# Kernel optimization log

Measured on AMD Instinct MI355X. Metric: run time of the kernel, lower is better.

## Reference

```python
import jax, jax.numpy as jnp
import numpy as np

B, N, C = 2, 2048, 768
H = 12
HD = C // H  # 64
EPS = 1e-6


def setup_inputs() -> dict:
    key = jax.random.key(0)
    ks = jax.random.split(key, 6)
    x = jax.random.normal(ks[0], (B, N, C), dtype=jnp.float32)
    # Xavier-uniform-ish init for kernels
    lim_qkv = float(np.sqrt(6.0 / (C + 3 * C)))
    lim_proj = float(np.sqrt(6.0 / (C + C)))
    qkv_kernel = jax.random.uniform(ks[1], (C, 3 * C), minval=-lim_qkv, maxval=lim_qkv, dtype=jnp.float32)
    qkv_bias = jnp.zeros((3 * C,), dtype=jnp.float32)
    proj_kernel = jax.random.uniform(ks[2], (C, C), minval=-lim_proj, maxval=lim_proj, dtype=jnp.float32)
    proj_bias = jnp.zeros((C,), dtype=jnp.float32)
    q_norm_w = jnp.ones((HD,), dtype=jnp.float32)
    k_norm_w = jnp.ones((HD,), dtype=jnp.float32)
    # Standard RoPE tables: freqs over half the head dim, tiled to full head_dim
    half = HD // 2
    inv_freq = 1.0 / (10000.0 ** (jnp.arange(0, half, dtype=jnp.float32) / half))
    t = jnp.arange(N, dtype=jnp.float32)
    freqs = jnp.outer(t, inv_freq)               # (N, HD/2)
    emb = jnp.concatenate([freqs, freqs], axis=-1)  # (N, HD)
    rope_cos = jnp.cos(emb)
    rope_sin = jnp.sin(emb)
    return {"x": x, "rope_cos": rope_cos, "rope_sin": rope_sin,
            "qkv_kernel": qkv_kernel, "qkv_bias": qkv_bias,
            "proj_kernel": proj_kernel, "proj_bias": proj_bias,
            "q_norm_w": q_norm_w, "k_norm_w": k_norm_w}


def _rms_norm(x, w):
    var = jnp.mean(x * x, axis=-1, keepdims=True)
    return x * jax.lax.rsqrt(var + EPS) * w


def _rope(x, cos, sin):
    # x: (B, H, N, HD); cos/sin: (N, HD)
    half = x.shape[-1] // 2
    x1, x2 = x[..., :half], x[..., half:]
    rot = jnp.concatenate([-x2, x1], axis=-1)
    return x * cos + rot * sin


def reference(x, rope_cos, rope_sin, qkv_kernel, qkv_bias, proj_kernel, proj_bias, q_norm_w, k_norm_w):
    b, n, c = x.shape
    qkv = x @ qkv_kernel + qkv_bias                       # (B, N, 3C)
    qkv = qkv.reshape(b, n, 3, H, HD).transpose(2, 0, 3, 1, 4)  # (3, B, H, N, HD)
    q, k, v = qkv[0], qkv[1], qkv[2]
    q = _rope(_rms_norm(q, q_norm_w), rope_cos, rope_sin)
    k = _rope(_rms_norm(k, k_norm_w), rope_cos, rope_sin)
    scale = 1.0 / jnp.sqrt(jnp.float32(HD)).astype(x.dtype)
    attn = jnp.einsum('bhqd,bhkd->bhqk', q, k) * scale    # (B, H, N, N)
    attn = jax.nn.softmax(attn, axis=-1)
    out = jnp.einsum('bhqk,bhkd->bhqd', attn, v)          # (B, H, N, HD)
    out = out.swapaxes(1, 2).reshape(b, n, c)
    return out @ proj_kernel + proj_bias
```

## Files before the change

### kernel.cpp

```cpp
#include <hip/hip_runtime.h>
#include <math.h>

#define B_    2
#define N_    2048
#define C_    768
#define H_    12
#define HD_   64
#define NROWS (B_*N_)
#define QKVC  (3*C_)
#define EPSV  1e-6f
#define SCALE 0.125f
#define LOG2E 1.44269504088896f
#define SMAX  12.0f

typedef unsigned short u16;
typedef short bf16x8 __attribute__((ext_vector_type(8)));
typedef float f32x4  __attribute__((ext_vector_type(4)));

__device__ __forceinline__ float b2f(u16 u) {
    unsigned v = ((unsigned)u) << 16;
    return __builtin_bit_cast(float, v);
}
__device__ __forceinline__ u16 f2b(float f) {
    unsigned u = __builtin_bit_cast(unsigned, f);
    u += 0x7fffu + ((u >> 16) & 1u);
    return (u16)(u >> 16);
}
__device__ __forceinline__ unsigned pk2(float a, float b) {
#if __has_builtin(__builtin_amdgcn_cvt_pk_bf16_f32)
    auto r = __builtin_amdgcn_cvt_pk_bf16_f32(a, b);
    return __builtin_bit_cast(unsigned, r);
#else
    return (unsigned)f2b(a) | ((unsigned)f2b(b) << 16);
#endif
}
__device__ __forceinline__ float fexp2(float x) {
#if __has_builtin(__builtin_amdgcn_exp2f)
    return __builtin_amdgcn_exp2f(x);
#else
    return exp2f(x);
#endif
}
__device__ __forceinline__ void gload_lds16(const void* g, void* l) {
    __builtin_amdgcn_global_load_lds(
        (const __attribute__((address_space(1))) unsigned int*)g,
        (__attribute__((address_space(3))) unsigned int*)l, 16, 0, 0);
}

__global__ __launch_bounds__(256)
void cvt_bf16_kernel(const float* __restrict__ src, u16* __restrict__ dst) {
    const int i = (blockIdx.x * 256 + threadIdx.x) * 4;
    const float4 v = *(const float4*)(src + i);
    uint2 o = { pk2(v.x, v.y), pk2(v.z, v.w) };
    *(uint2*)(dst + i) = o;
}

__global__ __launch_bounds__(256)
void wtrans_kernel(const float* __restrict__ W, u16* __restrict__ Wt,
                   int K, int N) {
    __shared__ float T[64][65];
    const int k0 = blockIdx.y * 64, n0 = blockIdx.x * 64;
    const int t = threadIdx.x, r = t >> 6, c = t & 63;
#pragma unroll
    for (int p = 0; p < 16; ++p) {
        const int kl = p * 4 + r;
        T[kl][c] = W[(size_t)(k0 + kl) * N + n0 + c];
    }
    __syncthreads();
#pragma unroll
    for (int p = 0; p < 16; ++p) {
        const int nl = p * 4 + r;
        Wt[(size_t)(n0 + nl) * K + k0 + c] = f2b(T[c][nl]);
    }
}

template <bool BF16OUT, int BN>
__global__ __launch_bounds__(256)
void gemm_tn_kernel(const u16* __restrict__ A, const u16* __restrict__ Bt,
                    const float* __restrict__ bias, void* __restrict__ Cout,
                    int M, int N, int K) {
    constexpr int NB = BN / 32;
    __shared__ __attribute__((aligned(16))) u16 As[128 * 32];
    __shared__ __attribute__((aligned(16))) u16 Bs[BN * 32];
    const int tid = threadIdx.x;
    const int w = tid >> 6, l = tid & 63;
    const int lq = l & 15, quad = l >> 4;

    const int gx  = gridDim.x;
    const int nwg = gx * gridDim.y;
    const int d   = blockIdx.x + gx * blockIdx.y;
    const int lin = (d & 7) * (nwg >> 3) + (d >> 3);
    const int mbase = (lin / gx) * 128, nbase = (lin % gx) * BN;

    f32x4 acc[4][NB];
    const f32x4 z4 = {0.f, 0.f, 0.f, 0.f};
#pragma unroll
    for (int mb = 0; mb < 4; ++mb)
#pragma unroll
        for (int nb = 0; nb < NB; ++nb) acc[mb][nb] = z4;

    const int srow = (l >> 2);
    const int sdc  = (l & 3) ^ ((l >> 2) & 3);

    for (int k0 = 0; k0 < K; k0 += 32) {
#pragma unroll
        for (int cc = 0; cc < 2; ++cc) {
            const int c = 2 * w + cc;
            const int row = 16 * c + srow;
            gload_lds16(A + (size_t)(mbase + row) * K + k0 + sdc * 8, &As[c * 512]);
        }
#pragma unroll
        for (int cc = 0; cc < BN / 64; ++cc) {
            const int c = (BN / 64) * w + cc;
            const int row = 16 * c + srow;
            gload_lds16(Bt + (size_t)(nbase + row) * K + k0 + sdc * 8, &Bs[c * 512]);
        }
        __syncthreads();

        bf16x8 af[4], bfr[NB];
#pragma unroll
        for (int mb = 0; mb < 4; ++mb)
            af[mb] = *(const bf16x8*)
                &As[((w >> 1) * 64 + mb * 16 + lq) * 32 + ((quad ^ (lq & 3)) * 8)];
#pragma unroll
        for (int nb = 0; nb < NB; ++nb)
            bfr[nb] = *(const bf16x8*)
                &Bs[((w & 1) * (BN / 2) + nb * 16 + lq) * 32 + ((quad ^ (lq & 3)) * 8)];
#pragma unroll
        for (int mb = 0; mb < 4; ++mb)
#pragma unroll
            for (int nb = 0; nb < NB; ++nb)
                acc[mb][nb] = __builtin_amdgcn_mfma_f32_16x16x32_bf16(
                    af[mb], bfr[nb], acc[mb][nb], 0, 0, 0);
        __syncthreads();
    }

#pragma unroll
    for (int nb = 0; nb < NB; ++nb) {
        const int col = nbase + (w & 1) * (BN / 2) + nb * 16 + lq;
        const float bv = bias[col];
#pragma unroll
        for (int mb = 0; mb < 4; ++mb) {
#pragma unroll
            for (int r = 0; r < 4; ++r) {
                const int row = mbase + (w >> 1) * 64 + mb * 16 + quad * 4 + r;
                const float v = acc[mb][nb][r] + bv;
                if (BF16OUT) ((u16*)Cout)[(size_t)row * N + col] = f2b(v);
                else         ((float*)Cout)[(size_t)row * N + col] = v;
            }
        }
    }
}

__global__ __launch_bounds__(256)
void normrope_kernel(u16* __restrict__ qkv, u16* __restrict__ kpack,
                     const float* __restrict__ cosb,
                     const float* __restrict__ sinb,
                     const float* __restrict__ qw,
                     const float* __restrict__ kw) {
    const int item = blockIdx.x * 16 + (threadIdx.x >> 4);
    const int lq   = threadIdx.x & 15;
    const int h    = item % H_;
    const int row  = item / H_;
    const int n    = row & (N_ - 1);
    const int b    = row >> 11;
    const size_t base = (size_t)row * QKVC + h * HD_ + lq * 4;

    const ushort4 q4 = *(const ushort4*)&qkv[base];
    const ushort4 k4 = *(const ushort4*)&qkv[base + C_];
    float qf[4], kf[4];
    qf[0] = b2f(q4.x); qf[1] = b2f(q4.y); qf[2] = b2f(q4.z); qf[3] = b2f(q4.w);
    kf[0] = b2f(k4.x); kf[1] = b2f(k4.y); kf[2] = b2f(k4.z); kf[3] = b2f(k4.w);

    float q2 = qf[0]*qf[0] + qf[1]*qf[1] + qf[2]*qf[2] + qf[3]*qf[3];
    float k2 = kf[0]*kf[0] + kf[1]*kf[1] + kf[2]*kf[2] + kf[3]*kf[3];
#pragma unroll
    for (int off = 8; off >= 1; off >>= 1) {
        q2 += __shfl_xor(q2, off, 64);
        k2 += __shfl_xor(k2, off, 64);
    }
    const float rq = rsqrtf(q2 * (1.f / 64.f) + EPSV);
    const float rk = rsqrtf(k2 * (1.f / 64.f) + EPSV);

    const float4 qwv = *(const float4*)&qw[lq * 4];
    const float4 kwv = *(const float4*)&kw[lq * 4];
    const float4 cv  = *(const float4*)&cosb[n * HD_ + lq * 4];
    const float4 sv  = *(const float4*)&sinb[n * HD_ + lq * 4];

    float qn[4], kn[4];
    qn[0] = qf[0]*rq*qwv.x; qn[1] = qf[1]*rq*qwv.y;
    qn[2] = qf[2]*rq*qwv.z; qn[3] = qf[3]*rq*qwv.w;
    kn[0] = kf[0]*rk*kwv.x; kn[1] = kf[1]*rk*kwv.y;
    kn[2] = kf[2]*rk*kwv.z; kn[3] = kf[3]*rk*kwv.w;

    const float sgn = (lq < 8) ? -1.f : 1.f;
    float qo[4], ko[4];
    const float cc[4] = {cv.x, cv.y, cv.z, cv.w};
    const float ss[4] = {sv.x, sv.y, sv.z, sv.w};
#pragma unroll
    for (int j = 0; j < 4; ++j) {
        const float qp = __shfl_xor(qn[j], 8, 64);
        const float kp = __shfl_xor(kn[j], 8, 64);
        qo[j] = (qn[j] * cc[j] + sgn * qp * ss[j]) * (SCALE * LOG2E);
        ko[j] =  kn[j] * cc[j] + sgn * kp * ss[j];
    }
    uint2 qout = { pk2(qo[0], qo[1]), pk2(qo[2], qo[3]) };
    uint2 kout = { pk2(ko[0], ko[1]), pk2(ko[2], ko[3]) };
    *(uint2*)&qkv[base] = qout;

    const int kt = n >> 6, kr = n & 63;
    const int kb = kr >> 4, m = kr & 15;
    const int ks = lq >> 3, quad = (lq >> 1) & 3, jj = (lq & 1) * 4;
    const size_t off = ((size_t)(b * H_ + h) * 32 + kt) * 4096
                     + (size_t)((kb * 2 + ks) * 64 + quad * 16 + m) * 8 + jj;
    *(uint2*)&kpack[off] = kout;
}

__global__ __launch_bounds__(256)
void vpack_kernel(const u16* __restrict__ qkv, u16* __restrict__ vpack) {
    __shared__ u16 Tv[64][72];
    const int kt = blockIdx.x, bh = blockIdx.y;
    const int b = bh / H_, h = bh % H_;
    const int t = threadIdx.x;
    {
        const int r = t >> 2, seg = t & 3;
        const u16* src = &qkv[(size_t)(b * N_ + kt * 64 + r) * QKVC
                              + 2 * C_ + h * HD_ + seg * 16];
        const uint4 v0 = *(const uint4*)src;
        const uint4 v1 = *(const uint4*)(src + 8);
        *(uint4*)&Tv[r][seg * 16]     = v0;
        *(uint4*)&Tv[r][seg * 16 + 8] = v1;
    }
    __syncthreads();
    u16 tmp[16];
#pragma unroll
    for (int g2 = 0; g2 < 2; ++g2) {
        const int g = t * 2 + g2;
        const int mbks = g >> 6;
        const int l  = g & 63;
        const int mb = mbks >> 1, ks = mbks & 1;
        const int m  = l & 15,  quad = l >> 4;
#pragma unroll
        for (int j = 0; j < 8; ++j)
            tmp[g2 * 8 + j] = Tv[ks * 32 + quad * 8 + j][mb * 16 + m];
    }
    u16* dst = &vpack[((size_t)bh * 32 + kt) * 4096 + t * 16];
    *(uint4*)dst       = *(const uint4*)&tmp[0];
    *(uint4*)(dst + 8) = *(const uint4*)&tmp[8];
}

#define NQ_   2
#define QB_   (NQ_ * 16)
#define NQT_  (N_ / QB_)

__global__ __launch_bounds__(128, 3)
void flash_mfma_kernel(const u16* __restrict__ qkv,
                       const u16* __restrict__ kpack,
                       const u16* __restrict__ vpack,
                       u16* __restrict__ attnb) {
    __shared__ __attribute__((aligned(16))) u16 Ps[2][QB_ * 64];
    __shared__ __attribute__((aligned(16))) float Oex[QB_ * 64];
    __shared__ float lex[QB_];

    const int tid = threadIdx.x;
    const int w = tid >> 6, l = tid & 63;
    const int lq = l & 15, quad = l >> 4;
    const int sw = lq & 7;

    const int lin  = blockIdx.x;
    const int slot = lin >> 3;
    const int bh   = (lin & 7) * 3 + (slot / NQT_);
    const int qt   = slot & (NQT_ - 1);
    const int b = bh / H_, h = bh % H_;
    const size_t qbase = (size_t)b * N_ * QKVC + h * HD_;
    const size_t tbase = (size_t)bh * 32 * 4096;

    bf16x8 qb[NQ_][2];
#pragma unroll
    for (int nq = 0; nq < NQ_; ++nq)
#pragma unroll
        for (int ks = 0; ks < 2; ++ks)
            qb[nq][ks] = *(const bf16x8*)
                &qkv[qbase + (size_t)(qt * QB_ + nq * 16 + lq) * QKVC
                     + ks * 32 + quad * 8];

    float lsum[NQ_];
#pragma unroll
    for (int nq = 0; nq < NQ_; ++nq) lsum[nq] = 0.f;
    f32x4 oacc[4][NQ_];
    const f32x4 z4 = {0.f, 0.f, 0.f, 0.f};
#pragma unroll
    for (int mb = 0; mb < 4; ++mb)
#pragma unroll
        for (int nq = 0; nq < NQ_; ++nq) oacc[mb][nq] = z4;

    bf16x8 ka[4][2];
#pragma unroll
    for (int kb = 0; kb < 4; ++kb)
#pragma unroll
        for (int ks = 0; ks < 2; ++ks)
            ka[kb][ks] = *(const bf16x8*)
                &kpack[tbase + (size_t)w * 4096 + ((kb * 2 + ks) * 64 + l) * 8];

    for (int kt2 = 0; kt2 < 16; ++kt2) {
        const int kt  = 2 * kt2 + w;
        const int ktn = (kt + 2) & 31;
        const size_t vb = tbase + (size_t)kt * 4096;
        const size_t kb_n = tbase + (size_t)ktn * 4096;

        bf16x8 va[4][2];
#pragma unroll
        for (int mb = 0; mb < 4; ++mb)
#pragma unroll
            for (int ks = 0; ks < 2; ++ks)
                va[mb][ks] = *(const bf16x8*)
                    &vpack[vb + ((mb * 2 + ks) * 64 + l) * 8];

#pragma unroll
        for (int kb = 0; kb < 4; ++kb) {
            f32x4 sacc[NQ_];
#pragma unroll
            for (int nq = 0; nq < NQ_; ++nq) sacc[nq] = z4;
            __builtin_amdgcn_s_setprio(1);
#pragma unroll
            for (int ks = 0; ks < 2; ++ks)
#pragma unroll
                for (int nq = 0; nq < NQ_; ++nq)
                    sacc[nq] = __builtin_amdgcn_mfma_f32_16x16x32_bf16(
                        ka[kb][ks], qb[nq][ks], sacc[nq], 0, 0, 0);
            __builtin_amdgcn_s_setprio(0);
#pragma unroll
            for (int nq = 0; nq < NQ_; ++nq) {
                float p[4];
#pragma unroll
                for (int r = 0; r < 4; ++r) p[r] = fexp2(sacc[nq][r] - SMAX);
                lsum[nq] += (p[0] + p[1]) + (p[2] + p[3]);
                uint2 pkv = { pk2(p[0], p[1]), pk2(p[2], p[3]) };
                *(uint2*)&Ps[w][(nq * 16 + lq) * 64
                                + (((kb * 2 + (quad >> 1)) ^ sw) * 8)
                                + (quad & 1) * 4] = pkv;
            }
        }

#pragma unroll
        for (int kb = 0; kb < 4; ++kb)
#pragma unroll
            for (int ks = 0; ks < 2; ++ks)
                ka[kb][ks] = *(const bf16x8*)
                    &kpack[kb_n + ((kb * 2 + ks) * 64 + l) * 8];

        bf16x8 pb[2][NQ_];
#pragma unroll
        for (int ks = 0; ks < 2; ++ks)
#pragma unroll
            for (int nq = 0; nq < NQ_; ++nq)
                pb[ks][nq] = *(const bf16x8*)
                    &Ps[w][(nq * 16 + lq) * 64 + (((ks * 4 + quad) ^ sw) * 8)];

        __builtin_amdgcn_s_setprio(1);
#pragma unroll
        for (int mb = 0; mb < 4; ++mb)
#pragma unroll
            for (int ks = 0; ks < 2; ++ks)
#pragma unroll
                for (int nq = 0; nq < NQ_; ++nq)
                    oacc[mb][nq] = __builtin_amdgcn_mfma_f32_16x16x32_bf16(
                        va[mb][ks], pb[ks][nq], oacc[mb][nq], 0, 0, 0);
        __builtin_amdgcn_s_setprio(0);
    }

#pragma unroll
    for (int nq = 0; nq < NQ_; ++nq) {
        lsum[nq] += __shfl_xor(lsum[nq], 16, 64);
        lsum[nq] += __shfl_xor(lsum[nq], 32, 64);
    }

    if (w == 1) {
#pragma unroll
        for (int nq = 0; nq < NQ_; ++nq) {
#pragma unroll
            for (int mb = 0; mb < 4; ++mb) {
                const int chunk = (mb * 4 + quad) ^ lq;
                *(float4*)&Oex[(nq * 16 + lq) * 64 + chunk * 4] =
                    *(float4*)&oacc[mb][nq];
            }
            if (quad == 0) lex[nq * 16 + lq] = lsum[nq];
        }
    }
    __syncthreads();
    if (w == 0) {
#pragma unroll
        for (int nq = 0; nq < NQ_; ++nq) {
            const int qrow = nq * 16 + lq;
            const float inv = 1.f / (lsum[nq] + lex[qrow]);
#pragma unroll
            for (int mb = 0; mb < 4; ++mb) {
                const int chunk = (mb * 4 + quad) ^ lq;
                const float4 oe = *(const float4*)&Oex[qrow * 64 + chunk * 4];
                const float o0 = (oacc[mb][nq][0] + oe.x) * inv;
                const float o1 = (oacc[mb][nq][1] + oe.y) * inv;
                const float o2 = (oacc[mb][nq][2] + oe.z) * inv;
                const float o3 = (oacc[mb][nq][3] + oe.w) * inv;
                uint2 ov = { pk2(o0, o1), pk2(o2, o3) };
                *(uint2*)&Ps[0][qrow * 64
                                + (((mb * 2 + (quad >> 1)) ^ sw) * 8)
                                + (quad & 1) * 4] = ov;
            }
        }
#pragma unroll
        for (int pass = 0; pass < QB_ / 8; ++pass) {
            const int ql = pass * 8 + (l >> 3);
            const int c  = l & 7;
            const bf16x8 v = *(const bf16x8*)&Ps[0][ql * 64 + ((c ^ (ql & 7)) * 8)];
            const int query = qt * QB_ + ql;
            *(bf16x8*)&attnb[(size_t)(b * N_ + query) * C_ + h * HD_ + c * 8] = v;
        }
    }
}

extern "C" void kernel_launch(void* const* d_in, const int* in_sizes, int n_in,
                              void* d_out, int out_size, void* d_ws, size_t ws_size,
                              hipStream_t stream) {
    const float* x        = (const float*)d_in[0];
    const float* rope_cos = (const float*)d_in[1];
    const float* rope_sin = (const float*)d_in[2];
    const float* qkv_w    = (const float*)d_in[3];
    const float* qkv_b    = (const float*)d_in[4];
    const float* proj_w   = (const float*)d_in[5];
    const float* proj_b   = (const float*)d_in[6];
    const float* q_nw     = (const float*)d_in[7];
    const float* k_nw     = (const float*)d_in[8];
    float* out = (float*)d_out;

    u16* xb    = (u16*)d_ws;
    u16* qwt   = xb    + (size_t)NROWS * C_;
    u16* pwt   = qwt   + (size_t)QKVC * C_;
    u16* qkvb  = pwt   + (size_t)C_ * C_;
    u16* vpackb= qkvb  + (size_t)NROWS * QKVC;
    u16* attnb = vpackb+ (size_t)B_ * H_ * 32 * 4096;
    u16* kpackb= xb;

    cvt_bf16_kernel<<<dim3(NROWS * C_ / 1024), 256, 0, stream>>>(x, xb);
    wtrans_kernel<<<dim3(QKVC / 64, C_ / 64), 256, 0, stream>>>(qkv_w, qwt, C_, QKVC);
    wtrans_kernel<<<dim3(C_ / 64, C_ / 64), 256, 0, stream>>>(proj_w, pwt, C_, C_);

    gemm_tn_kernel<true, 128><<<dim3(QKVC / 128, NROWS / 128), 256, 0, stream>>>(
        xb, qwt, qkv_b, qkvb, NROWS, QKVC, C_);

    normrope_kernel<<<dim3(NROWS * H_ / 16), 256, 0, stream>>>(
        qkvb, kpackb, rope_cos, rope_sin, q_nw, k_nw);

    vpack_kernel<<<dim3(32, B_ * H_), 256, 0, stream>>>(qkvb, vpackb);

    flash_mfma_kernel<<<dim3(B_ * H_ * NQT_), 128, 0, stream>>>(
        qkvb, kpackb, vpackb, attnb);

    gemm_tn_kernel<false, 64><<<dim3(C_ / 64, NROWS / 128), 256, 0, stream>>>(
        attnb, pwt, proj_b, out, NROWS, C_, C_);
}
```

Before: 180.4 us.

## Merge prep and norm/vpack launches; double-buffer K tiles in flash loop

Folds the three preprocessing kernels (x cast plus two weight transposes) into one launch, and the normrope and vpack kernels into one launch, with work routed by block-index ranges. This removes launch gaps and lets independent small jobs share the GPU at once. The flash attention loop now keeps K fragments in a two-slot register buffer and issues the next tile's K load before the QK MFMAs, so the load can overlap compute. The cost is more vector registers per wave, which may reduce occupancy under the 3-blocks-per-SM launch bound.

```diff
diff --git a/kernel.cpp b/kernel.cpp
--- a/kernel.cpp
+++ b/kernel.cpp
@@ -47,19 +47,11 @@
         (__attribute__((address_space(3))) unsigned int*)l, 16, 0, 0);
 }
 
-__global__ __launch_bounds__(256)
-void cvt_bf16_kernel(const float* __restrict__ src, u16* __restrict__ dst) {
-    const int i = (blockIdx.x * 256 + threadIdx.x) * 4;
-    const float4 v = *(const float4*)(src + i);
-    uint2 o = { pk2(v.x, v.y), pk2(v.z, v.w) };
-    *(uint2*)(dst + i) = o;
-}
-
-__global__ __launch_bounds__(256)
-void wtrans_kernel(const float* __restrict__ W, u16* __restrict__ Wt,
-                   int K, int N) {
-    __shared__ float T[64][65];
-    const int k0 = blockIdx.y * 64, n0 = blockIdx.x * 64;
+__device__ __forceinline__ void wtrans_body(const float* __restrict__ W,
+                                            u16* __restrict__ Wt,
+                                            int K, int N, int bx, int by,
+                                            float (*T)[65]) {
+    const int k0 = by * 64, n0 = bx * 64;
     const int t = threadIdx.x, r = t >> 6, c = t & 63;
 #pragma unroll
     for (int p = 0; p < 16; ++p) {
@@ -71,6 +63,25 @@
     for (int p = 0; p < 16; ++p) {
         const int nl = p * 4 + r;
         Wt[(size_t)(n0 + nl) * K + k0 + c] = f2b(T[c][nl]);
+    }
+}
+
+__global__ __launch_bounds__(256)
+void prep_kernel(const float* __restrict__ x, u16* __restrict__ xb,
+                 const float* __restrict__ qkv_w, u16* __restrict__ qwt,
+                 const float* __restrict__ proj_w, u16* __restrict__ pwt) {
+    __shared__ float T[64][65];
+    const int blk = blockIdx.x;
+    if (blk < 432) {
+        wtrans_body(qkv_w, qwt, C_, QKVC, blk % 36, blk / 36, T);
+    } else if (blk < 576) {
+        const int lin = blk - 432;
+        wtrans_body(proj_w, pwt, C_, C_, lin % 12, lin / 12, T);
+    } else {
+        const int i = ((blk - 576) * 256 + threadIdx.x) * 4;
+        const float4 v = *(const float4*)(x + i);
+        uint2 o = { pk2(v.x, v.y), pk2(v.z, v.w) };
+        *(uint2*)(xb + i) = o;
     }
 }
 
@@ -152,13 +163,12 @@
     }
 }
 
-__global__ __launch_bounds__(256)
-void normrope_kernel(u16* __restrict__ qkv, u16* __restrict__ kpack,
-                     const float* __restrict__ cosb,
-                     const float* __restrict__ sinb,
-                     const float* __restrict__ qw,
-                     const float* __restrict__ kw) {
-    const int item = blockIdx.x * 16 + (threadIdx.x >> 4);
+__device__ __forceinline__ void normrope_body(
+        u16* __restrict__ qkv, u16* __restrict__ kpack,
+        const float* __restrict__ cosb, const float* __restrict__ sinb,
+        const float* __restrict__ qw, const float* __restrict__ kw,
+        int blk) {
+    const int item = blk * 16 + (threadIdx.x >> 4);
     const int lq   = threadIdx.x & 15;
     const int h    = item % H_;
     const int row  = item / H_;
@@ -216,10 +226,9 @@
     *(uint2*)&kpack[off] = kout;
 }
 
-__global__ __launch_bounds__(256)
-void vpack_kernel(const u16* __restrict__ qkv, u16* __restrict__ vpack) {
-    __shared__ u16 Tv[64][72];
-    const int kt = blockIdx.x, bh = blockIdx.y;
+__device__ __forceinline__ void vpack_body(
+        const u16* __restrict__ qkv, u16* __restrict__ vpack,
+        int kt, int bh, u16 (*Tv)[72]) {
     const int b = bh / H_, h = bh % H_;
     const int t = threadIdx.x;
     {
@@ -249,6 +258,22 @@
     *(uint4*)(dst + 8) = *(const uint4*)&tmp[8];
 }
 
+__global__ __launch_bounds__(256)
+void normvpack_kernel(u16* __restrict__ qkv, u16* __restrict__ kpack,
+                      u16* __restrict__ vpack,
+                      const float* __restrict__ cosb,
+                      const float* __restrict__ sinb,
+                      const float* __restrict__ qw,
+                      const float* __restrict__ kw) {
+    __shared__ u16 Tv[64][72];
+    const int blk = blockIdx.x;
+    if (blk < 768) {
+        vpack_body(qkv, vpack, blk & 31, blk >> 5, Tv);
+    } else {
+        normrope_body(qkv, kpack, cosb, sinb, qw, kw, blk - 768);
+    }
+}
+
 #define NQ_   2
 #define QB_   (NQ_ * 16)
 #define NQT_  (N_ / QB_)
@@ -294,80 +319,89 @@
 #pragma unroll
         for (int nq = 0; nq < NQ_; ++nq) oacc[mb][nq] = z4;
 
-    bf16x8 ka[4][2];
+    bf16x8 ka[2][4][2];
 #pragma unroll
     for (int kb = 0; kb < 4; ++kb)
 #pragma unroll
         for (int ks = 0; ks < 2; ++ks)
-            ka[kb][ks] = *(const bf16x8*)
+            ka[0][kb][ks] = *(const bf16x8*)
                 &kpack[tbase + (size_t)w * 4096 + ((kb * 2 + ks) * 64 + l) * 8];
 
-    for (int kt2 = 0; kt2 < 16; ++kt2) {
-        const int kt  = 2 * kt2 + w;
-        const int ktn = (kt + 2) & 31;
-        const size_t vb = tbase + (size_t)kt * 4096;
-        const size_t kb_n = tbase + (size_t)ktn * 4096;
-
-        bf16x8 va[4][2];
-#pragma unroll
-        for (int mb = 0; mb < 4; ++mb)
-#pragma unroll
-            for (int ks = 0; ks < 2; ++ks)
-                va[mb][ks] = *(const bf16x8*)
-                    &vpack[vb + ((mb * 2 + ks) * 64 + l) * 8];
-
-#pragma unroll
-        for (int kb = 0; kb < 4; ++kb) {
-            f32x4 sacc[NQ_];
-#pragma unroll
-            for (int nq = 0; nq < NQ_; ++nq) sacc[nq] = z4;
-            __builtin_amdgcn_s_setprio(1);
-#pragma unroll
-            for (int ks = 0; ks < 2; ++ks)
-#pragma unroll
-                for (int nq = 0; nq < NQ_; ++nq)
-                    sacc[nq] = __builtin_amdgcn_mfma_f32_16x16x32_bf16(
-                        ka[kb][ks], qb[nq][ks], sacc[nq], 0, 0, 0);
-            __builtin_amdgcn_s_setprio(0);
-#pragma unroll
-            for (int nq = 0; nq < NQ_; ++nq) {
-                float p[4];
-#pragma unroll
-                for (int r = 0; r < 4; ++r) p[r] = fexp2(sacc[nq][r] - SMAX);
-                lsum[nq] += (p[0] + p[1]) + (p[2] + p[3]);
-                uint2 pkv = { pk2(p[0], p[1]), pk2(p[2], p[3]) };
-                *(uint2*)&Ps[w][(nq * 16 + lq) * 64
-                                + (((kb * 2 + (quad >> 1)) ^ sw) * 8)
-                                + (quad & 1) * 4] = pkv;
-            }
-        }
-
-#pragma unroll
-        for (int kb = 0; kb < 4; ++kb)
-#pragma unroll
-            for (int ks = 0; ks < 2; ++ks)
-                ka[kb][ks] = *(const bf16x8*)
-                    &kpack[kb_n + ((kb * 2 + ks) * 64 + l) * 8];
-
-        bf16x8 pb[2][NQ_];
-#pragma unroll
-        for (int ks = 0; ks < 2; ++ks)
-#pragma unroll
-            for (int nq = 0; nq < NQ_; ++nq)
-                pb[ks][nq] = *(const bf16x8*)
-                    &Ps[w][(nq * 16 + lq) * 64 + (((ks * 4 + quad) ^ sw) * 8)];
-
-        __builtin_amdgcn_s_setprio(1);
-#pragma unroll
-        for (int mb = 0; mb < 4; ++mb)
-#pragma unroll
-            for (int ks = 0; ks < 2; ++ks)
-#pragma unroll
-                for (int nq = 0; nq < NQ_; ++nq)
-                    oacc[mb][nq] = __builtin_amdgcn_mfma_f32_16x16x32_bf16(
-                        va[mb][ks], pb[ks][nq], oacc[mb][nq], 0, 0, 0);
-        __builtin_amdgcn_s_setprio(0);
-    }
+    int kt2i = 0;
+
+#define FLASH_ITER(P)                                                         \
+    do {                                                                      \
+        const int kt  = 2 * kt2i + w;                                         \
+        const int ktn = (kt + 2) & 31;         \
+        const size_t vb   = tbase + (size_t)kt * 4096;                        \
+        const size_t kb_n = tbase + (size_t)ktn * 4096;                       \
+             \
+        bf16x8 va[4][2];                                                      \
+        _Pragma("unroll")                                                     \
+        for (int mb = 0; mb < 4; ++mb)                                        \
+            _Pragma("unroll")                                                 \
+            for (int ks = 0; ks < 2; ++ks)                                    \
+                va[mb][ks] = *(const bf16x8*)                                 \
+                    &vpack[vb + ((mb * 2 + ks) * 64 + l) * 8];                \
+        _Pragma("unroll")                                                     \
+        for (int kb = 0; kb < 4; ++kb)                                        \
+            _Pragma("unroll")                                                 \
+            for (int ks = 0; ks < 2; ++ks)                                    \
+                ka[1 - (P)][kb][ks] = *(const bf16x8*)                        \
+                    &kpack[kb_n + ((kb * 2 + ks) * 64 + l) * 8];              \
+                                      \
+        _Pragma("unroll")                                                     \
+        for (int kb = 0; kb < 4; ++kb) {                                      \
+            f32x4 sacc[NQ_];                                                  \
+            _Pragma("unroll")                                                 \
+            for (int nq = 0; nq < NQ_; ++nq) sacc[nq] = z4;                   \
+            __builtin_amdgcn_s_setprio(1);                                    \
+            _Pragma("unroll")                                                 \
+            for (int ks = 0; ks < 2; ++ks)                                    \
+                _Pragma("unroll")                                             \
+                for (int nq = 0; nq < NQ_; ++nq)                              \
+                    sacc[nq] = __builtin_amdgcn_mfma_f32_16x16x32_bf16(       \
+                        ka[(P)][kb][ks], qb[nq][ks], sacc[nq], 0, 0, 0);      \
+            __builtin_amdgcn_s_setprio(0);                                    \
+            _Pragma("unroll")                                                 \
+            for (int nq = 0; nq < NQ_; ++nq) {                                \
+                float p[4];                                                   \
+                _Pragma("unroll")                                             \
+                for (int r = 0; r < 4; ++r) p[r] = fexp2(sacc[nq][r] - SMAX); \
+                lsum[nq] += (p[0] + p[1]) + (p[2] + p[3]);                    \
+                uint2 pkv = { pk2(p[0], p[1]), pk2(p[2], p[3]) };             \
+                *(uint2*)&Ps[w][(nq * 16 + lq) * 64                           \
+                                + (((kb * 2 + (quad >> 1)) ^ sw) * 8)         \
+                                + (quad & 1) * 4] = pkv;                      \
+            }                                                                 \
+        }                                                                     \
+              \
+        bf16x8 pb[2][NQ_];                                                    \
+        _Pragma("unroll")                                                     \
+        for (int ks = 0; ks < 2; ++ks)                                        \
+            _Pragma("unroll")                                                 \
+            for (int nq = 0; nq < NQ_; ++nq)                                  \
+                pb[ks][nq] = *(const bf16x8*)                                 \
+                    &Ps[w][(nq * 16 + lq) * 64 + (((ks * 4 + quad) ^ sw) * 8)];\
+                                                          \
+        __builtin_amdgcn_s_setprio(1);                                        \
+        _Pragma("unroll")                                                     \
+        for (int mb = 0; mb < 4; ++mb)                                        \
+            _Pragma("unroll")                                                 \
+            for (int ks = 0; ks < 2; ++ks)                                    \
+                _Pragma("unroll")                                             \
+                for (int nq = 0; nq < NQ_; ++nq)                              \
+                    oacc[mb][nq] = __builtin_amdgcn_mfma_f32_16x16x32_bf16(   \
+                        va[mb][ks], pb[ks][nq], oacc[mb][nq], 0, 0, 0);       \
+        __builtin_amdgcn_s_setprio(0);                                        \
+        ++kt2i;                                                               \
+    } while (0)
+
+    for (int it8 = 0; it8 < 8; ++it8) {
+        FLASH_ITER(0);
+        FLASH_ITER(1);
+    }
+#undef FLASH_ITER
 
 #pragma unroll
     for (int nq = 0; nq < NQ_; ++nq) {
@@ -440,17 +474,14 @@
     u16* attnb = vpackb+ (size_t)B_ * H_ * 32 * 4096;
     u16* kpackb= xb;
 
-    cvt_bf16_kernel<<<dim3(NROWS * C_ / 1024), 256, 0, stream>>>(x, xb);
-    wtrans_kernel<<<dim3(QKVC / 64, C_ / 64), 256, 0, stream>>>(qkv_w, qwt, C_, QKVC);
-    wtrans_kernel<<<dim3(C_ / 64, C_ / 64), 256, 0, stream>>>(proj_w, pwt, C_, C_);
+    prep_kernel<<<dim3(576 + NROWS * C_ / 1024), 256, 0, stream>>>(
+        x, xb, qkv_w, qwt, proj_w, pwt);
 
     gemm_tn_kernel<true, 128><<<dim3(QKVC / 128, NROWS / 128), 256, 0, stream>>>(
         xb, qwt, qkv_b, qkvb, NROWS, QKVC, C_);
 
-    normrope_kernel<<<dim3(NROWS * H_ / 16), 256, 0, stream>>>(
-        qkvb, kpackb, rope_cos, rope_sin, q_nw, k_nw);
-
-    vpack_kernel<<<dim3(32, B_ * H_), 256, 0, stream>>>(qkvb, vpackb);
+    normvpack_kernel<<<dim3(768 + NROWS * H_ / 16), 256, 0, stream>>>(
+        qkvb, kpackb, vpackb, rope_cos, rope_sin, q_nw, k_nw);
 
     flash_mfma_kernel<<<dim3(B_ * H_ * NQT_), 128, 0, stream>>>(
         qkvb, kpackb, vpackb, attnb);
```

Result: slower. 215.3 us (+19.3%).
